# Kernel tuning notes

Hardware: AMD Instinct MI355X
Metric: run time of the kernel (lower is better)

Reference implementation:

```python
import jax, jax.numpy as jnp
import numpy as np

B, L, D = 16, 1024, 1024
OUT_LEN = 24
N_LAYERS = 3
CYCLE = L
LN_EPS = 1e-5


def _make_pe(seq_len, hidden, cycle):
    # pe[t, j] = 2*pi*t/cycle, then sin on even cols, cos on odd cols
    t = jnp.arange(seq_len, dtype=jnp.float32)[:, None]
    base = (2.0 * jnp.pi * t / cycle) * jnp.ones((1, hidden), jnp.float32)
    cols = jnp.arange(hidden)
    return jnp.where((cols % 2 == 0)[None, :], jnp.sin(base), jnp.cos(base))


def setup_inputs() -> dict:
    key = jax.random.key(0)
    ks = jax.random.split(key, 12)
    s = 0.02
    return {
        "x": jax.random.normal(ks[0], (B, L, D), jnp.float32),
        "pe": _make_pe(L, D, CYCLE),
        "w1": jax.random.normal(ks[1], (N_LAYERS, D, D), jnp.float32) * s,
        "b1": jnp.zeros((N_LAYERS, D), jnp.float32),
        "w2": jax.random.normal(ks[2], (N_LAYERS, D, D), jnp.float32) * s,
        "b2": jnp.zeros((N_LAYERS, D), jnp.float32),
        "ln_g": jnp.ones((N_LAYERS, D), jnp.float32),
        "ln_b": jnp.zeros((N_LAYERS, D), jnp.float32),
        "fc_w": jax.random.normal(ks[3], (1, D), jnp.float32) * s,
        "fc_b": jnp.zeros((1,), jnp.float32),
        "final_w": jax.random.normal(ks[4], (OUT_LEN, L), jnp.float32) * s,
        "final_b": jnp.zeros((OUT_LEN,), jnp.float32),
    }


def _layer_norm(y, g, b):
    mu = jnp.mean(y, axis=-1, keepdims=True)
    var = jnp.mean((y - mu) ** 2, axis=-1, keepdims=True)
    return (y - mu) * jax.lax.rsqrt(var + LN_EPS) * g + b


def reference(x, pe, w1, b1, w2, b2, ln_g, ln_b, fc_w, fc_b, final_w, final_b):
    d = x.shape[-1]
    scale = 1.0 / jnp.sqrt(jnp.float32(d))
    # positional add (pe[:, :seq_len]; here L == D so this is the full buffer)
    h = x + pe[:, : x.shape[1]]
    attns = []
    for l in range(w1.shape[0]):
        # hand-rolled bmm-softmax-bmm self-attention (q = k = v = h)
        scores = jnp.einsum("bqd,bkd->bqk", h, h) * scale  # (B, L, L)
        a = jax.nn.softmax(scores, axis=-1)
        ctx = jnp.einsum("bqk,bkd->bqd", a, h)
        # position-wise FFN with hidden == D, residual over ctx, then LN
        ff = jnp.maximum(ctx @ w1[l].T + b1[l], 0.0) @ w2[l].T + b2[l]
        h = _layer_norm(ctx + ff, ln_g[l], ln_b[l])
        attns.append(a)
    # final head: D -> 1, squeeze, then L -> OUT_LEN over the sequence dim
    z = (h @ fc_w.T + fc_b)[..., 0]  # (B, L)
    out = z @ final_w.T + final_b    # (B, OUT_LEN)
    return (out, jnp.stack(attns))
```

## Files before the change

### kernel.cpp

```cpp
#include <hip/hip_runtime.h>

typedef unsigned short u16;
typedef __attribute__((ext_vector_type(8))) short short8;
typedef __attribute__((ext_vector_type(4))) float f32x4;
typedef __attribute__((ext_vector_type(4))) unsigned short u16x4;

__device__ __forceinline__ float bf2f(u16 u){
  union { unsigned int i; float f; } x; x.i = ((unsigned int)u) << 16; return x.f;
}
__device__ __forceinline__ u16 f2bf(float f){
  union { float f; unsigned int i; } x; x.f = f;
  return (u16)((x.i + 0x7fffu + ((x.i >> 16) & 1u)) >> 16);
}
__device__ __forceinline__ void async16(const void* g, void* s){
  __builtin_amdgcn_global_load_lds((const __attribute__((address_space(1))) void*)g,
                                   (__attribute__((address_space(3))) void*)s, 16, 0, 0);
}

__global__ __launch_bounds__(256) void k_split2(const float* __restrict__ s1, u16* __restrict__ d1,
                                                const float* __restrict__ s2, u16* __restrict__ d2){
  long i = ((long)blockIdx.x * 256 + threadIdx.x) * 4;
  f32x4 v1 = *(const f32x4*)(s1 + i);
  f32x4 v2 = *(const f32x4*)(s2 + i);
  u16x4 h1, h2;
  #pragma unroll
  for (int j=0;j<4;j++){ h1[j] = f2bf(v1[j]); h2[j] = f2bf(v2[j]); }
  *(u16x4*)(d1+i) = h1;
  *(u16x4*)(d2+i) = h2;
}

__global__ __launch_bounds__(256) void k_addpe(const float* __restrict__ x, const float* __restrict__ pe,
                                               u16* __restrict__ d){
  long i = ((long)blockIdx.x * 256 + threadIdx.x) * 4;
  f32x4 xv = *(const f32x4*)(x + i);
  f32x4 pv = *(const f32x4*)(pe + (i & 1048575));
  u16x4 hh;
  #pragma unroll
  for (int j=0;j<4;j++) hh[j] = f2bf(xv[j]+pv[j]);
  *(u16x4*)(d+i) = hh;
}

__global__ __launch_bounds__(256) void k_transpose(const u16* __restrict__ in, u16* __restrict__ outp){
  __shared__ u16 tile[64][68];
  const long b = blockIdx.z;
  const int d0 = blockIdx.x * 64, l0 = blockIdx.y * 64;
  const long ibase = b * 1048576l;
  const int t = threadIdx.x;
  const int cr = t >> 4;
  const int cc = (t & 15) * 4;
  #pragma unroll
  for (int rr=0; rr<4; rr++){
    int row = cr + rr*16;
    u16x4 v = *(const u16x4*)(in + ibase + (long)(l0+row)*1024 + d0 + cc);
    *(u16x4*)&tile[row][cc] = v;
  }
  __syncthreads();
  #pragma unroll
  for (int rr=0; rr<4; rr++){
    int drow = cr + rr*16;
    u16x4 y;
    y[0] = tile[cc+0][drow];
    y[1] = tile[cc+1][drow];
    y[2] = tile[cc+2][drow];
    y[3] = tile[cc+3][drow];
    *(u16x4*)(outp + ibase + (long)(d0+drow)*1024 + l0 + cc) = y;
  }
}

template<int MODE>
__global__ __launch_bounds__(512, 2) void gemm8(
    const u16* __restrict__ aB, const u16* __restrict__ bB,
    int per, long sA, long sB, long sC,
    int lda, int ldb, int ldc,
    float scale, const float* __restrict__ bias,
    const u16* __restrict__ res,
    float* __restrict__ cF, u16* __restrict__ cB)
{
  __shared__ __align__(16) u16 sm[65536];
  const int t = threadIdx.x;
  const int w = t >> 6, lane = t & 63;
  const int wm = w >> 2, wn = w & 3;
  const int fr = lane & 15, fs = lane >> 4;

  const int p = blockIdx.x;
  const int chunk = gridDim.x >> 3;
  const int id = (p & 7) * chunk + (p >> 3);
  const long bz = id / per;
  const int rem = id % per;
  const int m0 = (rem >> 2) << 8, n0 = (rem & 3) << 8;

  const u16* a = aB + bz * sA;
  const u16* b = bB + bz * sB;

  const int urow = t >> 2;
  const int col8 = ((t & 3) ^ ((t >> 3) & 3)) * 8;
  const u16* gA0 = a + (long)(m0 + urow) * lda + col8;
  const u16* gA1 = a + (long)(m0 + 128 + urow) * lda + col8;
  const u16* gB0 = b + (long)(n0 + urow) * ldb + col8;
  const u16* gB1 = b + (long)(n0 + 128 + urow) * ldb + col8;
  u16* dA0 = sm + (w << 9);
  u16* dA1 = sm + 4096 + (w << 9);
  u16* dB0 = sm + 8192 + (w << 9);
  u16* dB1 = sm + 12288 + (w << 9);

  int offA[8], offB[4];
  #pragma unroll
  for (int i=0;i<8;i++){
    int row = wm*128 + i*16 + fr;
    int sl = fs ^ ((row >> 1) & 3);
    offA[i] = row*32 + sl*8;
  }
  #pragma unroll
  for (int j=0;j<4;j++){
    int row = wn*64 + j*16 + fr;
    int sl = fs ^ ((row >> 1) & 3);
    offB[j] = 8192 + row*32 + sl*8;
  }

  f32x4 acc[8][4];
  #pragma unroll
  for (int i=0;i<8;i++)
    #pragma unroll
    for (int j=0;j<4;j++) acc[i][j] = (f32x4){0.f,0.f,0.f,0.f};

  #pragma unroll
  for (int pb=0; pb<3; ++pb){
    const int kb = pb*32, sb = pb*16384;
    async16(gA0+kb, dA0+sb); async16(gA1+kb, dA1+sb);
    async16(gB0+kb, dB0+sb); async16(gB1+kb, dB1+sb);
  }
  gA0 += 96; gA1 += 96; gB0 += 96; gB1 += 96;
  asm volatile("s_waitcnt vmcnt(8)" ::: "memory");
  __builtin_amdgcn_s_barrier();
  __builtin_amdgcn_sched_barrier(0);

#define KT_BODY(SMB)                                                           \
    short8 aF[8], bF[4];                                                       \
    _Pragma("unroll")                                                          \
    for (int i=0;i<8;i++) aF[i] = *(const short8*)((SMB) + offA[i]);           \
    _Pragma("unroll")                                                          \
    for (int j=0;j<4;j++) bF[j] = *(const short8*)((SMB) + offB[j]);           \
    __builtin_amdgcn_s_barrier();                                              \
    __builtin_amdgcn_sched_barrier(0);                                         \
    __builtin_amdgcn_s_setprio(1);                                             \
    _Pragma("unroll")                                                          \
    for (int i=0;i<8;i++){                                                     \
      acc[i][0] = __builtin_amdgcn_mfma_f32_16x16x32_bf16(aF[i], bF[0], acc[i][0], 0,0,0); \
      acc[i][1] = __builtin_amdgcn_mfma_f32_16x16x32_bf16(aF[i], bF[1], acc[i][1], 0,0,0); \
    }                                                                          \
    _Pragma("unroll")                                                          \
    for (int i=0;i<8;i++){                                                     \
      acc[i][2] = __builtin_amdgcn_mfma_f32_16x16x32_bf16(aF[i], bF[2], acc[i][2], 0,0,0); \
      acc[i][3] = __builtin_amdgcn_mfma_f32_16x16x32_bf16(aF[i], bF[3], acc[i][3], 0,0,0); \
    }                                                                          \
    __builtin_amdgcn_s_setprio(0);

  for (int kt = 0; kt < 29; ++kt){
    const u16* smb = sm + (kt & 3)*16384;
    const int sb = ((kt + 3) & 3)*16384;
    async16(gA0, dA0+sb); async16(gA1, dA1+sb);
    async16(gB0, dB0+sb); async16(gB1, dB1+sb);
    gA0 += 32; gA1 += 32; gB0 += 32; gB1 += 32;
    KT_BODY(smb)
    asm volatile("s_waitcnt vmcnt(8)" ::: "memory");
    __builtin_amdgcn_s_barrier();
    __builtin_amdgcn_sched_barrier(0);
  }
  {
    const u16* smb = sm + (29 & 3)*16384;
    KT_BODY(smb)
    asm volatile("s_waitcnt vmcnt(4)" ::: "memory");
    __builtin_amdgcn_s_barrier();
    __builtin_amdgcn_sched_barrier(0);
  }
  {
    const u16* smb = sm + (30 & 3)*16384;
    KT_BODY(smb)
    asm volatile("s_waitcnt vmcnt(0)" ::: "memory");
    __builtin_amdgcn_s_barrier();
    __builtin_amdgcn_sched_barrier(0);
  }
  {
    const u16* smb = sm + (31 & 3)*16384;
    KT_BODY(smb)
  }
#undef KT_BODY

  const long cBase = bz * sC;
  const int rb = m0 + wm*128 + fs*4;
  const int cb = n0 + wn*64 + fr;
  #pragma unroll
  for (int j=0;j<4;j++){
    const int c = cb + j*16;
    float bv = 0.f;
    if constexpr (MODE == 2 || MODE == 3) bv = bias[c];
    #pragma unroll
    for (int i=0;i<8;i++){
      #pragma unroll
      for (int q=0;q<4;q++){
        const int r = rb + i*16 + q;
        const long idx = cBase + (long)r*ldc + c;
        float v = acc[i][j][q];
        if constexpr (MODE == 0){
          cF[idx] = v * scale;
        } else if constexpr (MODE == 1){
          cB[idx] = f2bf(v);
        } else if constexpr (MODE == 2){
          cB[idx] = f2bf(fmaxf(v + bv, 0.f));
        } else {
          cF[idx] = v + bv + bf2f(res[idx]);
        }
      }
    }
  }
}

__global__ __launch_bounds__(256) void k_softmax(float* __restrict__ p, u16* __restrict__ pB){
  const long row = blockIdx.x;
  float* pr = p + row * 1024;
  const int t = threadIdx.x, w = t >> 6, lane = t & 63;
  __shared__ float rA[4], rB[4];
  f32x4 v = *(const f32x4*)(pr + t*4);
  float m = fmaxf(fmaxf(v[0],v[1]), fmaxf(v[2],v[3]));
  #pragma unroll
  for (int off=32; off; off>>=1) m = fmaxf(m, __shfl_xor(m, off));
  if (lane==0) rA[w] = m;
  __syncthreads();
  m = fmaxf(fmaxf(rA[0],rA[1]), fmaxf(rA[2],rA[3]));
  float e[4]; float s = 0.f;
  #pragma unroll
  for (int j=0;j<4;j++){ e[j] = expf(v[j]-m); s += e[j]; }
  #pragma unroll
  for (int off=32; off; off>>=1) s += __shfl_xor(s, off);
  if (lane==0) rB[w] = s;
  __syncthreads();
  s = rB[0]+rB[1]+rB[2]+rB[3];
  const float inv = 1.0f / s;
  f32x4 o; u16x4 hh;
  #pragma unroll
  for (int j=0;j<4;j++){
    float pv = e[j]*inv; o[j] = pv; hh[j] = f2bf(pv);
  }
  *(f32x4*)(pr + t*4) = o;
  *(u16x4*)(pB + row*1024 + t*4) = hh;
}

__global__ __launch_bounds__(256) void k_ln(const float* __restrict__ r,
                                            const float* __restrict__ g, const float* __restrict__ b,
                                            u16* __restrict__ h){
  const long row = blockIdx.x;
  const float* rr = r + row * 1024;
  const int t = threadIdx.x, w = t >> 6, lane = t & 63;
  __shared__ float rA[4], rB[4];
  f32x4 v = *(const f32x4*)(rr + t*4);
  float s = v[0]+v[1]+v[2]+v[3];
  #pragma unroll
  for (int off=32; off; off>>=1) s += __shfl_xor(s, off);
  if (lane==0) rA[w] = s;
  __syncthreads();
  const float mu = (rA[0]+rA[1]+rA[2]+rA[3]) * (1.0f/1024.0f);
  float sq = 0.f;
  #pragma unroll
  for (int j=0;j<4;j++){ float d = v[j]-mu; sq += d*d; }
  #pragma unroll
  for (int off=32; off; off>>=1) sq += __shfl_xor(sq, off);
  if (lane==0) rB[w] = sq;
  __syncthreads();
  const float var = (rB[0]+rB[1]+rB[2]+rB[3]) * (1.0f/1024.0f);
  const float inv = rsqrtf(var + 1e-5f);
  u16x4 hh;
  #pragma unroll
  for (int j=0;j<4;j++){
    int d = t*4+j;
    hh[j] = f2bf((v[j]-mu)*inv*g[d] + b[d]);
  }
  *(u16x4*)(h + row*1024 + t*4) = hh;
}

__global__ __launch_bounds__(256) void k_final1(const u16* __restrict__ h,
                                                const float* __restrict__ fw, const float* __restrict__ fb,
                                                float* __restrict__ z){
  const int row = blockIdx.x*4 + (threadIdx.x>>6);
  const int lane = threadIdx.x & 63;
  const long base = (long)row * 1024;
  const int d0 = lane * 16;
  float s = 0.f;
  #pragma unroll
  for (int j=0;j<16;j++){
    int d = d0 + j;
    s += bf2f(h[base+d]) * fw[d];
  }
  #pragma unroll
  for (int off=32; off; off>>=1) s += __shfl_xor(s, off);
  if (lane==0) z[row] = s + fb[0];
}

__global__ __launch_bounds__(256) void k_final2(const float* __restrict__ z,
                                                const float* __restrict__ fw, const float* __restrict__ fb,
                                                float* __restrict__ out){
  const int idx = blockIdx.x*4 + (threadIdx.x>>6);
  const int lane = threadIdx.x & 63;
  const int b = idx / 24, o = idx % 24;
  float s = 0.f;
  #pragma unroll
  for (int j=0;j<16;j++){
    int li = lane + j*64;
    s += z[b*1024 + li] * fw[o*1024 + li];
  }
  #pragma unroll
  for (int off=32; off; off>>=1) s += __shfl_xor(s, off);
  if (lane==0) out[idx] = s + fb[o];
}

extern "C" void kernel_launch(void* const* d_in, const int* in_sizes, int n_in,
                              void* d_out, int out_size, void* d_ws, size_t ws_size,
                              hipStream_t stream){
  const float* x   = (const float*)d_in[0];
  const float* pe  = (const float*)d_in[1];
  const float* w1  = (const float*)d_in[2];
  const float* b1  = (const float*)d_in[3];
  const float* w2  = (const float*)d_in[4];
  const float* b2  = (const float*)d_in[5];
  const float* lng = (const float*)d_in[6];
  const float* lnb = (const float*)d_in[7];
  const float* fcw = (const float*)d_in[8];
  const float* fcb = (const float*)d_in[9];
  const float* fw  = (const float*)d_in[10];
  const float* fb  = (const float*)d_in[11];
  float* out  = (float*)d_out;
  float* attn = out + 384;

  char* ws = (char*)d_ws;
  const long BB = 32l*1024*1024;
  u16* hB = (u16*)(ws + 0*BB);
  u16* tB = (u16*)(ws + 1*BB);
  u16* cB = (u16*)(ws + 2*BB);
  u16* pB = (u16*)(ws + 3*BB);
  float* rf = (float*)(ws + 4*BB);
  u16* w1B = (u16*)(ws + 6*BB);
  u16* w2B = w1B + 3l*1024*1024;
  float* z = (float*)(w2B + 3l*1024*1024);

  const long M1 = 1024l*1024;

  k_split2<<<3072, 256, 0, stream>>>(w1, w1B, w2, w2B);
  k_addpe<<<16384, 256, 0, stream>>>(x, pe, hB);
  k_transpose<<<dim3(16,16,16), 256, 0, stream>>>(hB, tB);

  for (int l = 0; l < 3; l++){
    float* sc = attn + (long)l*16*M1;
    gemm8<0><<<256, 512, 0, stream>>>(hB, hB, 16, M1,M1,M1, 1024,1024,1024,
        0.03125f, nullptr, nullptr, sc, nullptr);
    k_softmax<<<16384, 256, 0, stream>>>(sc, pB);
    gemm8<1><<<256, 512, 0, stream>>>(pB, tB, 16, M1,M1,M1, 1024,1024,1024,
        1.f, nullptr, nullptr, nullptr, cB);
    gemm8<2><<<256, 512, 0, stream>>>(cB, w1B+l*M1, 256, 0,0,0, 1024,1024,1024,
        1.f, b1+l*1024, nullptr, nullptr, pB);
    gemm8<3><<<256, 512, 0, stream>>>(pB, w2B+l*M1, 256, 0,0,0, 1024,1024,1024,
        1.f, b2+l*1024, cB, rf, nullptr);
    k_ln<<<16384, 256, 0, stream>>>(rf, lng+l*1024, lnb+l*1024, hB);
    if (l < 2) k_transpose<<<dim3(16,16,16), 256, 0, stream>>>(hB, tB);
  }

  k_final1<<<4096, 256, 0, stream>>>(hB, fcw, fcb, z);
  k_final2<<<96, 256, 0, stream>>>(z, fw, fb, out);
}
```

Baseline: 735.0 us.

## Fuse QK^T score GEMM with row softmax in one attention kernel

Replaces the separate score GEMM plus softmax kernel with a single kernel where each block computes a full 64x1024 row strip of scores in registers, then does max/sum reductions across waves via LDS and writes fp32 probabilities and bf16 copies directly. This removes the fp32 score write and re-read between the two kernels. In exchange the kernel uses occupancy 1 with a large accumulator set, and a 64-row strip per block changes the GEMM tiling and reuse.

```diff
diff --git a/kernel.cpp b/kernel.cpp
--- a/kernel.cpp
+++ b/kernel.cpp
@@ -65,6 +65,172 @@
     y[3] = tile[cc+3][drow];
     *(u16x4*)(outp + ibase + (long)(d0+drow)*1024 + l0 + cc) = y;
   }
+}
+
+__global__ __launch_bounds__(512, 1) void attn_sm(
+    const u16* __restrict__ hB, float* __restrict__ probs, u16* __restrict__ pB)
+{
+  __shared__ __align__(16) u16 sm[65536];
+  const int t = threadIdx.x;
+  const int w = t >> 6, lane = t & 63;
+  const int fr = lane & 15, fs = lane >> 4;
+
+  const int p = blockIdx.x;
+  const int id = (p & 7) * 32 + (p >> 3);
+  const long bz = id >> 4;
+  const int brow = (id & 15) << 6;
+
+  const u16* hb = hB + bz * 1048576l;
+
+  const u16* gsrc[8];
+  int gdst[8];
+  #pragma unroll
+  for (int c=0;c<8;c++){
+    int u = c*512 + t;
+    int row = u >> 2;
+    int slot = (u & 3) ^ ((row >> 1) & 3);
+    gsrc[c] = hb + (long)row*1024 + slot*8;
+    gdst[c] = c*4096 + w*512;
+  }
+
+  int offA[4], offB[8];
+  #pragma unroll
+  for (int i=0;i<4;i++){
+    int x = i*16 + fr;
+    offA[i] = (brow + x)*32 + (fs ^ (((brow + x)>>1)&3))*8;
+  }
+  #pragma unroll
+  for (int j=0;j<8;j++){
+    int x = w*128 + j*16 + fr;
+    offB[j] = x*32 + (fs ^ ((x>>1)&3))*8;
+  }
+
+  f32x4 acc[4][8];
+  #pragma unroll
+  for (int i=0;i<4;i++)
+    #pragma unroll
+    for (int j=0;j<8;j++) acc[i][j] = (f32x4){0.f,0.f,0.f,0.f};
+
+  #pragma unroll
+  for (int c=0;c<8;c++) async16(gsrc[c], sm + gdst[c]);
+  asm volatile("s_waitcnt vmcnt(0)" ::: "memory");
+  __builtin_amdgcn_s_barrier();
+  __builtin_amdgcn_sched_barrier(0);
+
+#define ATT_BODY(BUF)                                                          \
+    short8 aF[4], bF[8];                                                       \
+    _Pragma("unroll")                                                          \
+    for (int i=0;i<4;i++) aF[i] = *(const short8*)((BUF) + offA[i]);           \
+    _Pragma("unroll")                                                          \
+    for (int j=0;j<8;j++) bF[j] = *(const short8*)((BUF) + offB[j]);           \
+    __builtin_amdgcn_s_setprio(1);                                             \
+    _Pragma("unroll")                                                          \
+    for (int i=0;i<4;i++)                                                      \
+      _Pragma("unroll")                                                        \
+      for (int j=0;j<8;j++)                                                    \
+        acc[i][j] = __builtin_amdgcn_mfma_f32_16x16x32_bf16(aF[i], bF[j], acc[i][j], 0,0,0); \
+    __builtin_amdgcn_s_setprio(0);
+
+  for (int kt = 0; kt < 31; ++kt){
+    const u16* buf = sm + (kt & 1)*32768;
+    u16* stg = sm + ((kt + 1) & 1)*32768;
+    const int ko = (kt + 1)*32;
+    #pragma unroll
+    for (int c=0;c<8;c++) async16(gsrc[c] + ko, stg + gdst[c]);
+    ATT_BODY(buf)
+    asm volatile("s_waitcnt vmcnt(0)" ::: "memory");
+    __builtin_amdgcn_s_barrier();
+    __builtin_amdgcn_sched_barrier(0);
+  }
+  {
+    const u16* buf = sm + 32768;
+    ATT_BODY(buf)
+  }
+#undef ATT_BODY
+
+  float* red = (float*)sm;
+  const float SC = 0.03125f;
+
+  float mx[4][4];
+  #pragma unroll
+  for (int i=0;i<4;i++)
+    #pragma unroll
+    for (int q=0;q<4;q++){
+      float m = acc[i][0][q];
+      #pragma unroll
+      for (int j=1;j<8;j++) m = fmaxf(m, acc[i][j][q]);
+      #pragma unroll
+      for (int d=1; d<16; d<<=1) m = fmaxf(m, __shfl_xor(m, d));
+      mx[i][q] = m;
+    }
+  if (fr == 0){
+    #pragma unroll
+    for (int i=0;i<4;i++)
+      #pragma unroll
+      for (int q=0;q<4;q++) red[(i*16 + fs*4 + q)*8 + w] = mx[i][q];
+  }
+  __syncthreads();
+  float M[4][4];
+  #pragma unroll
+  for (int i=0;i<4;i++)
+    #pragma unroll
+    for (int q=0;q<4;q++){
+      const int row = i*16 + fs*4 + q;
+      f32x4 a = *(const f32x4*)&red[row*8];
+      f32x4 b = *(const f32x4*)&red[row*8+4];
+      M[i][q] = fmaxf(fmaxf(fmaxf(a[0],a[1]),fmaxf(a[2],a[3])),
+                      fmaxf(fmaxf(b[0],b[1]),fmaxf(b[2],b[3])));
+    }
+  float sum[4][4];
+  #pragma unroll
+  for (int i=0;i<4;i++)
+    #pragma unroll
+    for (int q=0;q<4;q++){
+      float s = 0.f;
+      #pragma unroll
+      for (int j=0;j<8;j++){
+        float e = expf((acc[i][j][q] - M[i][q]) * SC);
+        acc[i][j][q] = e;
+        s += e;
+      }
+      #pragma unroll
+      for (int d=1; d<16; d<<=1) s += __shfl_xor(s, d);
+      sum[i][q] = s;
+    }
+  __syncthreads();
+  if (fr == 0){
+    #pragma unroll
+    for (int i=0;i<4;i++)
+      #pragma unroll
+      for (int q=0;q<4;q++) red[(i*16 + fs*4 + q)*8 + w] = sum[i][q];
+  }
+  __syncthreads();
+  float inv[4][4];
+  #pragma unroll
+  for (int i=0;i<4;i++)
+    #pragma unroll
+    for (int q=0;q<4;q++){
+      const int row = i*16 + fs*4 + q;
+      f32x4 a = *(const f32x4*)&red[row*8];
+      f32x4 b = *(const f32x4*)&red[row*8+4];
+      inv[i][q] = 1.0f / (a[0]+a[1]+a[2]+a[3]+b[0]+b[1]+b[2]+b[3]);
+    }
+
+  const long obase = bz * 1048576l;
+  #pragma unroll
+  for (int i=0;i<4;i++)
+    #pragma unroll
+    for (int q=0;q<4;q++){
+      const long rbase = obase + (long)(brow + i*16 + fs*4 + q)*1024;
+      const float iv = inv[i][q];
+      #pragma unroll
+      for (int j=0;j<8;j++){
+        const int col = w*128 + j*16 + fr;
+        const float pv = acc[i][j][q] * iv;
+        probs[rbase + col] = pv;
+        pB[rbase + col] = f2bf(pv);
+      }
+    }
 }
 
 template<int MODE>
@@ -201,9 +367,7 @@
         const int r = rb + i*16 + q;
         const long idx = cBase + (long)r*ldc + c;
         float v = acc[i][j][q];
-        if constexpr (MODE == 0){
-          cF[idx] = v * scale;
-        } else if constexpr (MODE == 1){
+        if constexpr (MODE == 1){
           cB[idx] = f2bf(v);
         } else if constexpr (MODE == 2){
           cB[idx] = f2bf(fmaxf(v + bv, 0.f));
@@ -213,36 +377,6 @@
       }
     }
   }
-}
-
-__global__ __launch_bounds__(256) void k_softmax(float* __restrict__ p, u16* __restrict__ pB){
-  const long row = blockIdx.x;
-  float* pr = p + row * 1024;
-  const int t = threadIdx.x, w = t >> 6, lane = t & 63;
-  __shared__ float rA[4], rB[4];
-  f32x4 v = *(const f32x4*)(pr + t*4);
-  float m = fmaxf(fmaxf(v[0],v[1]), fmaxf(v[2],v[3]));
-  #pragma unroll
-  for (int off=32; off; off>>=1) m = fmaxf(m, __shfl_xor(m, off));
-  if (lane==0) rA[w] = m;
-  __syncthreads();
-  m = fmaxf(fmaxf(rA[0],rA[1]), fmaxf(rA[2],rA[3]));
-  float e[4]; float s = 0.f;
-  #pragma unroll
-  for (int j=0;j<4;j++){ e[j] = expf(v[j]-m); s += e[j]; }
-  #pragma unroll
-  for (int off=32; off; off>>=1) s += __shfl_xor(s, off);
-  if (lane==0) rB[w] = s;
-  __syncthreads();
-  s = rB[0]+rB[1]+rB[2]+rB[3];
-  const float inv = 1.0f / s;
-  f32x4 o; u16x4 hh;
-  #pragma unroll
-  for (int j=0;j<4;j++){
-    float pv = e[j]*inv; o[j] = pv; hh[j] = f2bf(pv);
-  }
-  *(f32x4*)(pr + t*4) = o;
-  *(u16x4*)(pB + row*1024 + t*4) = hh;
 }
 
 __global__ __launch_bounds__(256) void k_ln(const float* __restrict__ r,
@@ -349,9 +483,7 @@
 
   for (int l = 0; l < 3; l++){
     float* sc = attn + (long)l*16*M1;
-    gemm8<0><<<256, 512, 0, stream>>>(hB, hB, 16, M1,M1,M1, 1024,1024,1024,
-        0.03125f, nullptr, nullptr, sc, nullptr);
-    k_softmax<<<16384, 256, 0, stream>>>(sc, pB);
+    attn_sm<<<256, 512, 0, stream>>>(hB, sc, pB);
     gemm8<1><<<256, 512, 0, stream>>>(pB, tB, 16, M1,M1,M1, 1024,1024,1024,
         1.f, nullptr, nullptr, nullptr, cB);
     gemm8<2><<<256, 512, 0, stream>>>(cB, w1B+l*M1, 256, 0,0,0, 1024,1024,1024,
```

Measured after the change: 737.7 us. No clear change (+0.4%).
